# Optimization experiments

Hardware: AMD Instinct MI355X
Metric: run time of the kernel (lower is better)

Reference implementation:

```python
import jax, jax.numpy as jnp
import numpy as np

B, L, D = 16, 2048, 128
GROUP = 16
NG = L // GROUP  # number of groups per batch
ALPHA = 0.5


def setup_inputs() -> dict:
    key = jax.random.key(0)
    k0, k1, k2 = jax.random.split(key, 3)
    x = jax.random.normal(k0, (B, L, D), dtype=jnp.float32)
    # per-batch permutation = gather indices (each position used exactly once)
    group_tensor = jax.vmap(lambda k: jax.random.permutation(k, L))(
        jax.random.split(k1, B)).astype(jnp.int32)
    ctxlens = jnp.full((B,), L, dtype=jnp.int32)
    W = jax.random.normal(k2, (2 * D,), dtype=jnp.float32) * (1.0 / np.sqrt(D))
    norm_alpha = jnp.ones((2,), dtype=jnp.float32)
    norm_gamma = jnp.ones((2 * D,), dtype=jnp.float32)
    norm_beta = jnp.zeros((2 * D,), dtype=jnp.float32)
    return {"x": x, "group_tensor": group_tensor, "ctxlens": ctxlens, "W": W,
            "norm_alpha": norm_alpha, "norm_gamma": norm_gamma, "norm_beta": norm_beta}


def _leaky_relu(v):
    return jnp.where(v >= 0, v, 0.01 * v)


def _ncn_forward(x, group_tensor, ctxlens, W, norm_alpha, norm_gamma, norm_beta):
    Bd, Ld, Dd = x.shape
    ng = Ld // GROUP
    Wi, Wj = W[:Dd], W[Dd:]
    a1, a2 = norm_alpha[0], norm_alpha[1]
    g1, g2 = norm_gamma[:Dd], norm_gamma[Dd:]
    b1, b2 = norm_beta[:Dd], norm_beta[Dd:]

    # gather x by group indices -> [B, NG, GROUP, D]
    xg = jnp.take_along_axis(x, group_tensor[:, :, None].astype(jnp.int32), axis=1)
    xg = xg.reshape(Bd, ng, GROUP, Dd)

    def step(carry, j):
        xi, xa = carry  # each [B, NG, GROUP, D]
        xj = jax.lax.dynamic_slice_in_dim(xi, j, 1, axis=2)  # [B, NG, 1, D]
        sim = jnp.einsum('bgnd,d->bgn', xi, Wi) \
            + jnp.einsum('bgd,d->bg', xj[:, :, 0, :], Wj)[:, :, None]  # [B,NG,GROUP]
        T = ALPHA * xi + (1.0 - ALPHA) * sim[..., None] * xj
        T_norm = g1 * jnp.tanh(a1 * T) + b1
        Fv = _leaky_relu(T_norm)
        xa = xa + Fv                               # ya = xa + F
        xi = xi + g2 * jnp.tanh(a2 * xa) + b2      # yi = xi + norm2(ya)
        return (xi, xa), None

    (yi, ya), _ = jax.lax.scan(step, (xg, jnp.zeros_like(xg)), jnp.arange(GROUP))

    # kernel only processes/stores a group if its start offset < ctxlen
    valid = (jnp.arange(ng, dtype=jnp.int32) * GROUP)[None, :] < ctxlens[:, None]
    yi = jnp.where(valid[:, :, None, None], yi, 0.0).reshape(Bd, Ld, Dd)
    ya = jnp.where(valid[:, :, None, None], ya, 0.0).reshape(Bd, Ld, Dd)

    # scatter back to original positions
    bidx = jnp.arange(Bd)[:, None]
    yi_out = jnp.zeros_like(x).at[bidx, group_tensor].set(yi)
    ya_out = jnp.zeros_like(x).at[bidx, group_tensor].set(ya)
    return yi_out, ya_out


def reference(x, group_tensor, ctxlens, W, norm_alpha, norm_gamma, norm_beta):
    return _ncn_forward(x, group_tensor, ctxlens, W, norm_alpha, norm_gamma, norm_beta)
```

## Files before the change

kernel.cpp:

```cpp
#include <hip/hip_runtime.h>

#define B_ 16
#define L_ 2048
#define D_ 128
#define GROUP_ 16
#define NG_ (L_ / GROUP_)
#define LOG2E_ 1.44269504088896340736f

typedef float v2 __attribute__((ext_vector_type(2)));

template<int CTRL>
__device__ __forceinline__ float dpp_add(float v) {
    int x = __builtin_amdgcn_update_dpp(0, __float_as_int(v), CTRL, 0xF, 0xF, false);
    return v + __int_as_float(x);
}
__device__ __forceinline__ float row16_sum(float v) {
    v = dpp_add<0xB1>(v);
    v = dpp_add<0x4E>(v);
    v = dpp_add<0x141>(v);
    v = dpp_add<0x140>(v);
    return v;
}

#define LGKM_BARRIER() asm volatile("s_waitcnt lgkmcnt(0)\n\ts_barrier" ::: "memory")

#define UPDATE_ROW(CXI, ZA, SIMV, SELFN)                                      \
    _Pragma("unroll")                                                         \
    for (int k = 0; k < 4; ++k) {                                             \
        v2 u  = __builtin_elementwise_fma(SIMV, xjv[k], CXI[k]);              \
        v2 r1 = (v2){__builtin_amdgcn_rcpf(__builtin_amdgcn_exp2f(u.x) + 1.0f),   \
                     __builtin_amdgcn_rcpf(__builtin_amdgcn_exp2f(u.y) + 1.0f)};  \
        v2 tnS = __builtin_elementwise_fma(G1S[k], r1, B1S[k]);               \
        v2 FvS = SELFN(tnS, tnS * leak);                                      \
        ZA[k] += FvS;                                                         \
        v2 r2 = (v2){__builtin_amdgcn_rcpf(__builtin_amdgcn_exp2f(ZA[k].x) + 1.0f), \
                     __builtin_amdgcn_rcpf(__builtin_amdgcn_exp2f(ZA[k].y) + 1.0f)}; \
        CXI[k] = __builtin_elementwise_fma(G2c[k], r2, CXI[k] + B2c[k]);      \
    }

#define STEP_LOOP(SELFN)                                                      \
    for (int j = 0; j < GROUP_; ++j) {                                        \
        const int p = j & 1;                                                  \
        v2 xjv[4];                                                            \
        {                                                                     \
            float4 tA = *(const float4*)&s_xj[p][d0];                         \
            float4 tB = *(const float4*)&s_xj[p][d0 + 4];                     \
            xjv[0] = (v2){tA.x, tA.y}; xjv[1] = (v2){tA.z, tA.w};             \
            xjv[2] = (v2){tB.x, tB.y}; xjv[3] = (v2){tB.z, tB.w};             \
        }                                                                     \
                            \
        v2 pjv = (v2){0.0f, 0.0f};                                            \
        _Pragma("unroll")                                                     \
        for (int k = 0; k < 4; ++k) pjv = __builtin_elementwise_fma(xjv[k], Wj[k], pjv); \
        v2 svA = pjv, svB = pjv;                                              \
        _Pragma("unroll")                                                     \
        for (int k = 0; k < 4; ++k) svA = __builtin_elementwise_fma(cxiA[k], Wi[k], svA); \
        _Pragma("unroll")                                                     \
        for (int k = 0; k < 4; ++k) svB = __builtin_elementwise_fma(cxiB[k], Wi[k], svB); \
        const float simA = row16_sum(svA.x + svA.y);                          \
        const float simB = row16_sum(svB.x + svB.y);                          \
        const v2 simAv = (v2){simA, simA};                                    \
        const v2 simBv = (v2){simB, simB};                                    \
        UPDATE_ROW(cxiA, zaA, simAv, SELFN)                                   \
        UPDATE_ROW(cxiB, zaB, simBv, SELFN)                                   \
        const int jn = j + 1;                                                 \
        if (jn < GROUP_ && rp == (jn & 7)) {                                  \
            if (jn & 8) {                                                     \
                float4 oA = {cxiB[0].x, cxiB[0].y, cxiB[1].x, cxiB[1].y};     \
                float4 oB = {cxiB[2].x, cxiB[2].y, cxiB[3].x, cxiB[3].y};     \
                *(float4*)&s_xj[p ^ 1][d0]     = oA;                          \
                *(float4*)&s_xj[p ^ 1][d0 + 4] = oB;                          \
            } else {                                                          \
                float4 oA = {cxiA[0].x, cxiA[0].y, cxiA[1].x, cxiA[1].y};     \
                float4 oB = {cxiA[2].x, cxiA[2].y, cxiA[3].x, cxiA[3].y};     \
                *(float4*)&s_xj[p ^ 1][d0]     = oA;                          \
                *(float4*)&s_xj[p ^ 1][d0 + 4] = oB;                          \
            }                                                                 \
        }                                                                     \
        LGKM_BARRIER();                                                       \
    }

__global__ __launch_bounds__(128)
__attribute__((amdgpu_waves_per_eu(4, 4)))
void ncn_kernel(
    const float* __restrict__ x,
    const int*   __restrict__ gt,
    const int*   __restrict__ ctxlens,
    const float* __restrict__ W,
    const float* __restrict__ nalpha,
    const float* __restrict__ ngamma,
    const float* __restrict__ nbeta,
    float* __restrict__ out)
{
    const int blk = blockIdx.x;
    const int b   = blk >> 7;
    const int g   = blk & (NG_ - 1);
    const int tid = threadIdx.x;
    const int rp  = tid >> 4;
    const int rl  = tid & 15;
    const int d0  = rl << 3;

    __shared__ float s_xj[2][D_];

    const float a1 = nalpha[0];
    const float a2 = nalpha[1];
    const float ca = -a1 * LOG2E_;
    const float S  = -2.0f * a2 * LOG2E_;
    const float inv_ca = 1.0f / ca;
    const bool  selMin = (S < 0.0f);

    v2 Wi[4], Wj[4], G1S[4], B1S[4], G2c[4], B2c[4];
    {
        float4 wA = *(const float4*)(W + d0);
        float4 wB = *(const float4*)(W + d0 + 4);
        float4 vA = *(const float4*)(W + D_ + d0);
        float4 vB = *(const float4*)(W + D_ + d0 + 4);
        Wi[0] = inv_ca * (v2){wA.x, wA.y}; Wi[1] = inv_ca * (v2){wA.z, wA.w};
        Wi[2] = inv_ca * (v2){wB.x, wB.y}; Wi[3] = inv_ca * (v2){wB.z, wB.w};
        Wj[0] = inv_ca * (v2){vA.x, vA.y}; Wj[1] = inv_ca * (v2){vA.z, vA.w};
        Wj[2] = inv_ca * (v2){vB.x, vB.y}; Wj[3] = inv_ca * (v2){vB.z, vB.w};

        float4 g1A = *(const float4*)(ngamma + d0);
        float4 g1B = *(const float4*)(ngamma + d0 + 4);
        float4 g2A = *(const float4*)(ngamma + D_ + d0);
        float4 g2B = *(const float4*)(ngamma + D_ + d0 + 4);
        float4 b1A = *(const float4*)(nbeta + d0);
        float4 b1B = *(const float4*)(nbeta + d0 + 4);
        float4 b2A = *(const float4*)(nbeta + D_ + d0);
        float4 b2B = *(const float4*)(nbeta + D_ + d0 + 4);

        v2 g1v[4] = {(v2){g1A.x,g1A.y},(v2){g1A.z,g1A.w},(v2){g1B.x,g1B.y},(v2){g1B.z,g1B.w}};
        v2 b1v[4] = {(v2){b1A.x,b1A.y},(v2){b1A.z,b1A.w},(v2){b1B.x,b1B.y},(v2){b1B.z,b1B.w}};
        v2 g2v[4] = {(v2){g2A.x,g2A.y},(v2){g2A.z,g2A.w},(v2){g2B.x,g2B.y},(v2){g2B.z,g2B.w}};
        v2 b2v[4] = {(v2){b2A.x,b2A.y},(v2){b2A.z,b2A.w},(v2){b2B.x,b2B.y},(v2){b2B.z,b2B.w}};
#pragma unroll
        for (int k = 0; k < 4; ++k) {
            G1S[k] = (S * 2.0f) * g1v[k];
            B1S[k] = S * (b1v[k] - g1v[k]);
            G2c[k] = (ca * 2.0f) * g2v[k];
            B2c[k] = ca * (b2v[k] - g2v[k]);
        }
    }

    const int lA   = g * GROUP_ + rp;
    const int tokA = gt[b * L_ + lA];
    const int tokB = gt[b * L_ + lA + 8];
    const float* xpA = x + ((size_t)(b * L_ + tokA)) * D_ + d0;
    const float* xpB = x + ((size_t)(b * L_ + tokB)) * D_ + d0;

    v2 cxiA[4], zaA[4], cxiB[4], zaB[4];
    {
        const v2 cav = (v2){ca, ca};
        float4 xA = *(const float4*)xpA;
        float4 xB = *(const float4*)(xpA + 4);
        cxiA[0] = cav * (v2){xA.x, xA.y}; cxiA[1] = cav * (v2){xA.z, xA.w};
        cxiA[2] = cav * (v2){xB.x, xB.y}; cxiA[3] = cav * (v2){xB.z, xB.w};
        float4 yA = *(const float4*)xpB;
        float4 yB = *(const float4*)(xpB + 4);
        cxiB[0] = cav * (v2){yA.x, yA.y}; cxiB[1] = cav * (v2){yA.z, yA.w};
        cxiB[2] = cav * (v2){yB.x, yB.y}; cxiB[3] = cav * (v2){yB.z, yB.w};
    }
#pragma unroll
    for (int k = 0; k < 4; ++k) { zaA[k] = (v2){0.0f, 0.0f}; zaB[k] = (v2){0.0f, 0.0f}; }

    if (rp == 0) {
        float4 oA = {cxiA[0].x, cxiA[0].y, cxiA[1].x, cxiA[1].y};
        float4 oB = {cxiA[2].x, cxiA[2].y, cxiA[3].x, cxiA[3].y};
        *(float4*)&s_xj[0][d0]     = oA;
        *(float4*)&s_xj[0][d0 + 4] = oB;
    }
    __syncthreads();

    const v2 leak = (v2){0.01f, 0.01f};

    if (selMin) {
        STEP_LOOP(__builtin_elementwise_min)
    } else {
        STEP_LOOP(__builtin_elementwise_max)
    }

    const float invS = 1.0f / S;
    const v2 invSv  = (v2){invS, invS};
    const v2 invCav = (v2){inv_ca, inv_ca};

    const bool valid = (g * GROUP_) < ctxlens[b];

    float* o1A = out + ((size_t)(b * L_ + tokA)) * D_ + d0;
    float* o1B = out + ((size_t)(b * L_ + tokB)) * D_ + d0;
    float* o2A = o1A + (size_t)B_ * L_ * D_;
    float* o2B = o1B + (size_t)B_ * L_ * D_;

    v2 yiA[4], yaA[4], yiB[4], yaB[4];
#pragma unroll
    for (int k = 0; k < 4; ++k) {
        yiA[k] = cxiA[k] * invCav; yaA[k] = zaA[k] * invSv;
        yiB[k] = cxiB[k] * invCav; yaB[k] = zaB[k] * invSv;
    }
    if (!valid) {
#pragma unroll
        for (int k = 0; k < 4; ++k) {
            yiA[k] = (v2){0,0}; yaA[k] = (v2){0,0};
            yiB[k] = (v2){0,0}; yaB[k] = (v2){0,0};
        }
    }

    float4 s1A = {yiA[0].x, yiA[0].y, yiA[1].x, yiA[1].y};
    float4 s1B = {yiA[2].x, yiA[2].y, yiA[3].x, yiA[3].y};
    float4 s2A = {yaA[0].x, yaA[0].y, yaA[1].x, yaA[1].y};
    float4 s2B = {yaA[2].x, yaA[2].y, yaA[3].x, yaA[3].y};
    *(float4*)o1A       = s1A;
    *(float4*)(o1A + 4) = s1B;
    *(float4*)o2A       = s2A;
    *(float4*)(o2A + 4) = s2B;

    float4 t1A = {yiB[0].x, yiB[0].y, yiB[1].x, yiB[1].y};
    float4 t1B = {yiB[2].x, yiB[2].y, yiB[3].x, yiB[3].y};
    float4 t2A = {yaB[0].x, yaB[0].y, yaB[1].x, yaB[1].y};
    float4 t2B = {yaB[2].x, yaB[2].y, yaB[3].x, yaB[3].y};
    *(float4*)o1B       = t1A;
    *(float4*)(o1B + 4) = t1B;
    *(float4*)o2B       = t2A;
    *(float4*)(o2B + 4) = t2B;
}

extern "C" void kernel_launch(void* const* d_in, const int* in_sizes, int n_in,
                              void* d_out, int out_size, void* d_ws, size_t ws_size,
                              hipStream_t stream) {
    const float* x  = (const float*)d_in[0];
    const int*   gt = (const int*)d_in[1];
    const int*   cl = (const int*)d_in[2];
    const float* W  = (const float*)d_in[3];
    const float* na = (const float*)d_in[4];
    const float* ng = (const float*)d_in[5];
    const float* nb = (const float*)d_in[6];
    float* out = (float*)d_out;

    ncn_kernel<<<B_ * NG_, 128, 0, stream>>>(x, gt, cl, W, na, ng, nb, out);
}
```

Measured before the change: 112.6 us.

## Process two groups per block with 256 threads, one row per thread per group

Each block now handles two adjacent groups with 256 threads. Each thread owns the same row index in both groups, so the group's 16 rows are spread across all 16 row slots instead of two rows per thread within one group. There are now two shared xj buffers, one per group, and the same thread writes both rows at each step. This halves the block count and removes the branch that chose which row to publish. In exchange each thread still carries two rows, the block is larger, and occupancy may shift under the fixed waves-per-eu hint.

Result: no change. 113.5 us (+0.8%).

```diff
diff --git a/kernel.cpp b/kernel.cpp
--- a/kernel.cpp
+++ b/kernel.cpp
@@ -24,10 +24,10 @@
 
 #define LGKM_BARRIER() asm volatile("s_waitcnt lgkmcnt(0)\n\ts_barrier" ::: "memory")
 
-#define UPDATE_ROW(CXI, ZA, SIMV, SELFN)                                      \
+#define UPD8(CXI, ZA, SIMV, XJV, SELFN)                                       \
     _Pragma("unroll")                                                         \
     for (int k = 0; k < 4; ++k) {                                             \
-        v2 u  = __builtin_elementwise_fma(SIMV, xjv[k], CXI[k]);              \
+        v2 u  = __builtin_elementwise_fma(SIMV, XJV[k], CXI[k]);              \
         v2 r1 = (v2){__builtin_amdgcn_rcpf(__builtin_amdgcn_exp2f(u.x) + 1.0f),   \
                      __builtin_amdgcn_rcpf(__builtin_amdgcn_exp2f(u.y) + 1.0f)};  \
         v2 tnS = __builtin_elementwise_fma(G1S[k], r1, B1S[k]);               \
@@ -41,46 +41,48 @@
 #define STEP_LOOP(SELFN)                                                      \
     for (int j = 0; j < GROUP_; ++j) {                                        \
         const int p = j & 1;                                                  \
-        v2 xjv[4];                                                            \
+        v2 xjA[4], xjB[4];                                                    \
         {                                                                     \
-            float4 tA = *(const float4*)&s_xj[p][d0];                         \
-            float4 tB = *(const float4*)&s_xj[p][d0 + 4];                     \
-            xjv[0] = (v2){tA.x, tA.y}; xjv[1] = (v2){tA.z, tA.w};             \
-            xjv[2] = (v2){tB.x, tB.y}; xjv[3] = (v2){tB.z, tB.w};             \
-        }                                                                     \
-                            \
-        v2 pjv = (v2){0.0f, 0.0f};                                            \
+            float4 tA = *(const float4*)&s_xj[0][p][d0];                      \
+            float4 tB = *(const float4*)&s_xj[0][p][d0 + 4];                  \
+            xjA[0] = (v2){tA.x, tA.y}; xjA[1] = (v2){tA.z, tA.w};             \
+            xjA[2] = (v2){tB.x, tB.y}; xjA[3] = (v2){tB.z, tB.w};             \
+            float4 uA = *(const float4*)&s_xj[1][p][d0];                      \
+            float4 uB = *(const float4*)&s_xj[1][p][d0 + 4];                  \
+            xjB[0] = (v2){uA.x, uA.y}; xjB[1] = (v2){uA.z, uA.w};             \
+            xjB[2] = (v2){uB.x, uB.y}; xjB[3] = (v2){uB.z, uB.w};             \
+        }                                                                     \
+        v2 svA = (v2){0.0f, 0.0f}, svB = (v2){0.0f, 0.0f};                    \
         _Pragma("unroll")                                                     \
-        for (int k = 0; k < 4; ++k) pjv = __builtin_elementwise_fma(xjv[k], Wj[k], pjv); \
-        v2 svA = pjv, svB = pjv;                                              \
+        for (int k = 0; k < 4; ++k) {                                         \
+            svA = __builtin_elementwise_fma(cxiA[k], Wi[k], svA);             \
+            svB = __builtin_elementwise_fma(cxiB[k], Wi[k], svB);             \
+        }                                                                     \
         _Pragma("unroll")                                                     \
-        for (int k = 0; k < 4; ++k) svA = __builtin_elementwise_fma(cxiA[k], Wi[k], svA); \
-        _Pragma("unroll")                                                     \
-        for (int k = 0; k < 4; ++k) svB = __builtin_elementwise_fma(cxiB[k], Wi[k], svB); \
+        for (int k = 0; k < 4; ++k) {                                         \
+            svA = __builtin_elementwise_fma(xjA[k], Wj[k], svA);              \
+            svB = __builtin_elementwise_fma(xjB[k], Wj[k], svB);              \
+        }                                                                     \
         const float simA = row16_sum(svA.x + svA.y);                          \
         const float simB = row16_sum(svB.x + svB.y);                          \
         const v2 simAv = (v2){simA, simA};                                    \
         const v2 simBv = (v2){simB, simB};                                    \
-        UPDATE_ROW(cxiA, zaA, simAv, SELFN)                                   \
-        UPDATE_ROW(cxiB, zaB, simBv, SELFN)                                   \
-        const int jn = j + 1;                                                 \
-        if (jn < GROUP_ && rp == (jn & 7)) {                                  \
-            if (jn & 8) {                                                     \
-                float4 oA = {cxiB[0].x, cxiB[0].y, cxiB[1].x, cxiB[1].y};     \
-                float4 oB = {cxiB[2].x, cxiB[2].y, cxiB[3].x, cxiB[3].y};     \
-                *(float4*)&s_xj[p ^ 1][d0]     = oA;                          \
-                *(float4*)&s_xj[p ^ 1][d0 + 4] = oB;                          \
-            } else {                                                          \
-                float4 oA = {cxiA[0].x, cxiA[0].y, cxiA[1].x, cxiA[1].y};     \
-                float4 oB = {cxiA[2].x, cxiA[2].y, cxiA[3].x, cxiA[3].y};     \
-                *(float4*)&s_xj[p ^ 1][d0]     = oA;                          \
-                *(float4*)&s_xj[p ^ 1][d0 + 4] = oB;                          \
-            }                                                                 \
+        UPD8(cxiA, zaA, simAv, xjA, SELFN)                                    \
+        UPD8(cxiB, zaB, simBv, xjB, SELFN)                                    \
+        if (j + 1 < GROUP_ && row == j + 1) {                                 \
+            float4 oA = {cxiA[0].x, cxiA[0].y, cxiA[1].x, cxiA[1].y};         \
+            float4 oB = {cxiA[2].x, cxiA[2].y, cxiA[3].x, cxiA[3].y};         \
+            *(float4*)&s_xj[0][p ^ 1][d0]     = oA;                           \
+            *(float4*)&s_xj[0][p ^ 1][d0 + 4] = oB;                           \
+            float4 qA = {cxiB[0].x, cxiB[0].y, cxiB[1].x, cxiB[1].y};         \
+            float4 qB = {cxiB[2].x, cxiB[2].y, cxiB[3].x, cxiB[3].y};         \
+            *(float4*)&s_xj[1][p ^ 1][d0]     = qA;                           \
+            *(float4*)&s_xj[1][p ^ 1][d0 + 4] = qB;                           \
         }                                                                     \
         LGKM_BARRIER();                                                       \
     }
 
-__global__ __launch_bounds__(128)
+__global__ __launch_bounds__(256)
 __attribute__((amdgpu_waves_per_eu(4, 4)))
 void ncn_kernel(
     const float* __restrict__ x,
@@ -93,14 +95,15 @@
     float* __restrict__ out)
 {
     const int blk = blockIdx.x;
-    const int b   = blk >> 7;
-    const int g   = blk & (NG_ - 1);
+    const int b   = blk >> 6;
+    const int gp  = blk & 63;
+    const int gA  = gp << 1;
     const int tid = threadIdx.x;
-    const int rp  = tid >> 4;
+    const int row = tid >> 4;
     const int rl  = tid & 15;
     const int d0  = rl << 3;
 
-    __shared__ float s_xj[2][D_];
+    __shared__ float s_xj[2][2][D_];
 
     const float a1 = nalpha[0];
     const float a2 = nalpha[1];
@@ -142,9 +145,9 @@
         }
     }
 
-    const int lA   = g * GROUP_ + rp;
+    const int lA   = gA * GROUP_ + row;
     const int tokA = gt[b * L_ + lA];
-    const int tokB = gt[b * L_ + lA + 8];
+    const int tokB = gt[b * L_ + lA + GROUP_];
     const float* xpA = x + ((size_t)(b * L_ + tokA)) * D_ + d0;
     const float* xpB = x + ((size_t)(b * L_ + tokB)) * D_ + d0;
 
@@ -163,11 +166,15 @@
 #pragma unroll
     for (int k = 0; k < 4; ++k) { zaA[k] = (v2){0.0f, 0.0f}; zaB[k] = (v2){0.0f, 0.0f}; }
 
-    if (rp == 0) {
+    if (row == 0) {
         float4 oA = {cxiA[0].x, cxiA[0].y, cxiA[1].x, cxiA[1].y};
         float4 oB = {cxiA[2].x, cxiA[2].y, cxiA[3].x, cxiA[3].y};
-        *(float4*)&s_xj[0][d0]     = oA;
-        *(float4*)&s_xj[0][d0 + 4] = oB;
+        *(float4*)&s_xj[0][0][d0]     = oA;
+        *(float4*)&s_xj[0][0][d0 + 4] = oB;
+        float4 qA = {cxiB[0].x, cxiB[0].y, cxiB[1].x, cxiB[1].y};
+        float4 qB = {cxiB[2].x, cxiB[2].y, cxiB[3].x, cxiB[3].y};
+        *(float4*)&s_xj[1][0][d0]     = qA;
+        *(float4*)&s_xj[1][0][d0 + 4] = qB;
     }
     __syncthreads();
 
@@ -180,43 +187,38 @@
     }
 
     const float invS = 1.0f / S;
-    const v2 invSv  = (v2){invS, invS};
-    const v2 invCav = (v2){inv_ca, inv_ca};
-
-    const bool valid = (g * GROUP_) < ctxlens[b];
+    const int   cl   = ctxlens[b];
+    const bool  validA = (gA * GROUP_) < cl;
+    const bool  validB = ((gA + 1) * GROUP_) < cl;
+    const float mAc = validA ? inv_ca : 0.0f;
+    const float mAs = validA ? invS   : 0.0f;
+    const float mBc = validB ? inv_ca : 0.0f;
+    const float mBs = validB ? invS   : 0.0f;
+    const v2 mAcv = (v2){mAc, mAc}, mAsv = (v2){mAs, mAs};
+    const v2 mBcv = (v2){mBc, mBc}, mBsv = (v2){mBs, mBs};
 
     float* o1A = out + ((size_t)(b * L_ + tokA)) * D_ + d0;
     float* o1B = out + ((size_t)(b * L_ + tokB)) * D_ + d0;
     float* o2A = o1A + (size_t)B_ * L_ * D_;
     float* o2B = o1B + (size_t)B_ * L_ * D_;
 
-    v2 yiA[4], yaA[4], yiB[4], yaB[4];
-#pragma unroll
-    for (int k = 0; k < 4; ++k) {
-        yiA[k] = cxiA[k] * invCav; yaA[k] = zaA[k] * invSv;
-        yiB[k] = cxiB[k] * invCav; yaB[k] = zaB[k] * invSv;
-    }
-    if (!valid) {
-#pragma unroll
-        for (int k = 0; k < 4; ++k) {
-            yiA[k] = (v2){0,0}; yaA[k] = (v2){0,0};
-            yiB[k] = (v2){0,0}; yaB[k] = (v2){0,0};
-        }
-    }
-
-    float4 s1A = {yiA[0].x, yiA[0].y, yiA[1].x, yiA[1].y};
-    float4 s1B = {yiA[2].x, yiA[2].y, yiA[3].x, yiA[3].y};
-    float4 s2A = {yaA[0].x, yaA[0].y, yaA[1].x, yaA[1].y};
-    float4 s2B = {yaA[2].x, yaA[2].y, yaA[3].x, yaA[3].y};
+    v2 y0 = cxiA[0] * mAcv, y1 = cxiA[1] * mAcv, y2 = cxiA[2] * mAcv, y3 = cxiA[3] * mAcv;
+    v2 z0 = zaA[0] * mAsv,  z1 = zaA[1] * mAsv,  z2 = zaA[2] * mAsv,  z3 = zaA[3] * mAsv;
+    float4 s1A = {y0.x, y0.y, y1.x, y1.y};
+    float4 s1B = {y2.x, y2.y, y3.x, y3.y};
+    float4 s2A = {z0.x, z0.y, z1.x, z1.y};
+    float4 s2B = {z2.x, z2.y, z3.x, z3.y};
     *(float4*)o1A       = s1A;
     *(float4*)(o1A + 4) = s1B;
     *(float4*)o2A       = s2A;
     *(float4*)(o2A + 4) = s2B;
 
-    float4 t1A = {yiB[0].x, yiB[0].y, yiB[1].x, yiB[1].y};
-    float4 t1B = {yiB[2].x, yiB[2].y, yiB[3].x, yiB[3].y};
-    float4 t2A = {yaB[0].x, yaB[0].y, yaB[1].x, yaB[1].y};
-    float4 t2B = {yaB[2].x, yaB[2].y, yaB[3].x, yaB[3].y};
+    v2 w0 = cxiB[0] * mBcv, w1 = cxiB[1] * mBcv, w2 = cxiB[2] * mBcv, w3 = cxiB[3] * mBcv;
+    v2 v0 = zaB[0] * mBsv,  v1 = zaB[1] * mBsv,  v2_ = zaB[2] * mBsv, v3 = zaB[3] * mBsv;
+    float4 t1A = {w0.x, w0.y, w1.x, w1.y};
+    float4 t1B = {w2.x, w2.y, w3.x, w3.y};
+    float4 t2A = {v0.x, v0.y, v1.x, v1.y};
+    float4 t2B = {v2_.x, v2_.y, v3.x, v3.y};
     *(float4*)o1B       = t1A;
     *(float4*)(o1B + 4) = t1B;
     *(float4*)o2B       = t2A;
@@ -235,5 +237,5 @@
     const float* nb = (const float*)d_in[6];
     float* out = (float*)d_out;
 
-    ncn_kernel<<<B_ * NG_, 128, 0, stream>>>(x, gt, cl, W, na, ng, nb, out);
-}
+    ncn_kernel<<<B_ * (NG_ / 2), 256, 0, stream>>>(x, gt, cl, W, na, ng, nb, out);
+}
```
